# Performance work log

Measured on AMD Instinct MI355X. Metric: run time of the kernel, lower is better.

Reference implementation:

```python
import jax, jax.numpy as jnp
import numpy as np

N_EMBD = 768
N_HEAD = 12
HEAD_SIZE = N_EMBD // N_HEAD  # 64
WINDOW = 64  # sliding_window_size
EPS = 1e-6


def _rmsnorm(x, g):
    xf = x.astype(jnp.float32)
    n = xf * jax.lax.rsqrt(jnp.mean(xf * xf, axis=-1, keepdims=True) + EPS)
    return n.astype(x.dtype) * g


def _gelu_tanh(x):
    c = jnp.sqrt(jnp.asarray(2.0 / jnp.pi, x.dtype))
    return 0.5 * x * (1.0 + jnp.tanh(c * (x + 0.044715 * x ** 3)))


def setup_inputs() -> dict:
    key = jax.random.key(0)
    ks = jax.random.split(key, 12)
    B, T = 8, 1024
    s = 0.02
    return {
        "x": jax.random.normal(ks[0], (B, T, N_EMBD), jnp.float32),
        "w_q": jax.random.normal(ks[1], (N_EMBD, N_HEAD, HEAD_SIZE), jnp.float32) * s,
        "w_k": jax.random.normal(ks[2], (N_EMBD, N_HEAD, HEAD_SIZE), jnp.float32) * s,
        "w_v": jax.random.normal(ks[3], (N_EMBD, N_HEAD, HEAD_SIZE), jnp.float32) * s,
        "w_proj": jax.random.normal(ks[4], (N_EMBD, N_EMBD), jnp.float32) * s,
        "b_proj": jnp.zeros((N_EMBD,), jnp.float32),
        "w_ff1": jax.random.normal(ks[5], (N_EMBD, 4 * N_EMBD), jnp.float32) * s,
        "b_ff1": jnp.zeros((4 * N_EMBD,), jnp.float32),
        "w_ff2": jax.random.normal(ks[6], (4 * N_EMBD, N_EMBD), jnp.float32) * s,
        "b_ff2": jnp.zeros((N_EMBD,), jnp.float32),
        "g1": jnp.ones((N_EMBD,), jnp.float32),
        "g2": jnp.ones((N_EMBD,), jnp.float32),
    }


def reference(x, w_q, w_k, w_v, w_proj, b_proj, w_ff1, b_ff1, w_ff2, b_ff2, g1, g2):
    B, T, C = x.shape
    # ---- multi-head sliding-window causal attention (eval: dropout = identity) ----
    h = _rmsnorm(x, g1)
    q = jnp.einsum("btc,chd->bhtd", h, w_q)
    k = jnp.einsum("btc,chd->bhtd", h, w_k)
    v = jnp.einsum("btc,chd->bhtd", h, w_v)
    scores = jnp.einsum("bhtd,bhsd->bhts", q, k) / jnp.sqrt(jnp.asarray(HEAD_SIZE, x.dtype))
    pos = jnp.arange(T)
    diff = pos[:, None] - pos[None, :]  # q_pos - k_pos
    mask = (diff < 0) | (diff >= WINDOW)  # causal + sliding window of 64
    scores = jnp.where(mask[None, None], jnp.asarray(-jnp.inf, scores.dtype), scores)
    attn = jax.nn.softmax(scores, axis=-1)
    out = jnp.einsum("bhts,bhsd->bhtd", attn, v)
    out = out.transpose(0, 2, 1, 3).reshape(B, T, C)  # concat heads
    x = x + out @ w_proj + b_proj
    # ---- feedforward ----
    h2 = _rmsnorm(x, g2)
    ff = _gelu_tanh(h2 @ w_ff1 + b_ff1) @ w_ff2 + b_ff2
    x = x + ff
    aux = jnp.asarray(0.0, jnp.float32)
    return (x, aux)
```

## Files before the change

kernel.cpp:

```cpp
#include <hip/hip_runtime.h>
#include <cstdint>

#define DEVI __device__ __forceinline__

typedef __bf16 bf16x8 __attribute__((ext_vector_type(8)));
typedef float  f32x4  __attribute__((ext_vector_type(4)));

DEVI unsigned short f2b(float f){
  unsigned u = __builtin_bit_cast(unsigned, f);
  unsigned r = u + 0x7FFF + ((u >> 16) & 1);
  return (unsigned short)(r >> 16);
}
DEVI float b2f(unsigned short s){
  unsigned u = ((unsigned)s) << 16;
  return __builtin_bit_cast(float, u);
}
DEVI float gelu_f(float x){
  float u = 0.7978845608028654f * (x + 0.044715f * x * x * x);
  float e = __expf(2.0f * u);
  return x * (1.0f - 1.0f / (e + 1.0f));
}
DEVI void gl_lds16(const unsigned short* g, unsigned short* l){
  __builtin_amdgcn_global_load_lds(
      (const __attribute__((address_space(1))) unsigned int*)g,
      (__attribute__((address_space(3))) unsigned int*)l, 16, 0, 0);
}

__global__ __launch_bounds__(256)
void transpose_f2b(const float* __restrict__ in, unsigned short* __restrict__ out,
                   int R, int C)
{
  __shared__ float tile[32][33];
  int nbx = C >> 5;
  int bx = blockIdx.x % nbx, by = blockIdx.x / nbx;
  int c0 = bx << 5, r0 = by << 5;
  int tx = threadIdx.x & 31, ty = threadIdx.x >> 5;
  #pragma unroll
  for (int j = 0; j < 32; j += 8)
    tile[ty + j][tx] = in[(size_t)(r0 + ty + j) * C + c0 + tx];
  __syncthreads();
  #pragma unroll
  for (int j = 0; j < 32; j += 8)
    out[(size_t)(c0 + ty + j) * R + r0 + tx] = f2b(tile[tx][ty + j]);
}

__global__ __launch_bounds__(256)
void rmsnorm_k(const float* __restrict__ x, const float* __restrict__ g,
               unsigned short* __restrict__ out)
{
  int wid = threadIdx.x >> 6, lane = threadIdx.x & 63;
  size_t row = (size_t)blockIdx.x * 4 + wid;
  const float* xr = x + row * 768;
  float4 v[3];
  float ss = 0.0f;
  #pragma unroll
  for (int c = 0; c < 3; c++){
    v[c] = *(const float4*)&xr[lane * 4 + c * 256];
    ss += v[c].x * v[c].x + v[c].y * v[c].y + v[c].z * v[c].z + v[c].w * v[c].w;
  }
  #pragma unroll
  for (int o = 32; o >= 1; o >>= 1) ss += __shfl_xor(ss, o);
  float rs = rsqrtf(ss * (1.0f / 768.0f) + 1e-6f);
  #pragma unroll
  for (int c = 0; c < 3; c++){
    const float4 gv = *(const float4*)&g[lane * 4 + c * 256];
    ushort4 o4;
    o4.x = f2b(v[c].x * rs * gv.x);
    o4.y = f2b(v[c].y * rs * gv.y);
    o4.z = f2b(v[c].z * rs * gv.z);
    o4.w = f2b(v[c].w * rs * gv.w);
    *(ushort4*)&out[row * 768 + lane * 4 + c * 256] = o4;
  }
}

template<int BM, bool BIAS, bool GELU_, bool RES, bool OUTF32>
__global__ __launch_bounds__(256, BM == 64 ? 3 : 2)
void gemm_db(const unsigned short* __restrict__ A, const unsigned short* __restrict__ Bt,
             const float* __restrict__ bias, const float* __restrict__ res,
             void* __restrict__ outp, int M, int N, int K)
{
  constexpr int MI = BM / 32;
  constexpr int AL = (BM * 8) / 256;
  __shared__ unsigned short sm[2][(BM + 128) * 64];

  int tid = threadIdx.x, wid = tid >> 6, lane = tid & 63;
  int la = lane & 15, hi = lane >> 4;
  int wm = wid >> 1, wn = wid & 1;
  int tiles_n = N >> 7;
  int bid = blockIdx.x;
  bid = (bid & 7) * (gridDim.x >> 3) + (bid >> 3);
  int m0 = (bid / tiles_n) * BM, n0 = (bid % tiles_n) << 7;
  int NT = K >> 6;

  f32x4 acc[MI][4] = {};

  auto stage = [&](unsigned short* buf, int kt){
    #pragma unroll
    for (int l = 0; l < AL; l++){
      int cb  = wid * (BM * 2) + l * 64;
      int idx = cb + lane;
      int row = idx >> 3, slot = idx & 7, sl2 = slot ^ (row & 7);
      gl_lds16(A + (size_t)(m0 + row) * K + kt + sl2 * 8, buf + cb * 8);
    }
    #pragma unroll
    for (int l = 0; l < 4; l++){
      int cb  = wid * 256 + l * 64;
      int idx = cb + lane;
      int row = idx >> 3, slot = idx & 7, sl2 = slot ^ (row & 7);
      gl_lds16(Bt + (size_t)(n0 + row) * K + kt + sl2 * 8, buf + BM * 64 + cb * 8);
    }
  };

  stage(sm[0], 0);
  asm volatile("s_waitcnt vmcnt(0)" ::: "memory");
  __builtin_amdgcn_s_barrier();

  for (int t = 0; t < NT; t++){
    const unsigned short* As = sm[t & 1];
    const unsigned short* Bs = sm[t & 1] + BM * 64;

    if (t + 1 < NT) stage(sm[(t + 1) & 1], (t + 1) << 6);

    bf16x8 afr[MI][2], bfr[4][2];
    #pragma unroll
    for (int mm = 0; mm < MI; mm++)
      #pragma unroll
      for (int kk = 0; kk < 2; kk++){
        int r = wm * (BM / 2) + mm * 16 + la;
        afr[mm][kk] = *(const bf16x8*)&As[r * 64 + (((kk * 4 + hi) ^ (r & 7))) * 8];
      }
    #pragma unroll
    for (int nn = 0; nn < 4; nn++)
      #pragma unroll
      for (int kk = 0; kk < 2; kk++){
        int r = wn * 64 + nn * 16 + la;
        bfr[nn][kk] = *(const bf16x8*)&Bs[r * 64 + (((kk * 4 + hi) ^ (r & 7))) * 8];
      }
    #pragma unroll
    for (int mm = 0; mm < MI; mm++)
      #pragma unroll
      for (int nn = 0; nn < 4; nn++)
        #pragma unroll
        for (int kk = 0; kk < 2; kk++)
          acc[mm][nn] = __builtin_amdgcn_mfma_f32_16x16x32_bf16(
              afr[mm][kk], bfr[nn][kk], acc[mm][nn], 0, 0, 0);

    asm volatile("s_waitcnt vmcnt(0)" ::: "memory");
    __builtin_amdgcn_s_barrier();
  }

  float* outF = (float*)outp;
  unsigned short* outB = (unsigned short*)outp;
  #pragma unroll
  for (int mm = 0; mm < MI; mm++){
    int rowb = m0 + wm * (BM / 2) + mm * 16 + hi * 4;
    #pragma unroll
    for (int nn = 0; nn < 4; nn++){
      int col = n0 + wn * 64 + nn * 16 + la;
      float bv = BIAS ? bias[col] : 0.0f;
      #pragma unroll
      for (int r = 0; r < 4; r++){
        float val = acc[mm][nn][r] + bv;
        if (GELU_) val = gelu_f(val);
        if (RES)   val += res[(size_t)(rowb + r) * N + col];
        size_t o = (size_t)(rowb + r) * N + col;
        if (OUTF32) outF[o] = val;
        else        outB[o] = f2b(val);
      }
    }
  }
}

__global__ __launch_bounds__(256)
void attn_k(const unsigned short* __restrict__ qkv, unsigned short* __restrict__ attn)
{
  __shared__ unsigned short Qs[64 * 72];
  __shared__ unsigned short Ks[128 * 72];
  __shared__ unsigned short Vt[64 * 136];
  __shared__ unsigned short Ps[4][16 * 136];

  int tid = threadIdx.x, wid = tid >> 6, lane = tid & 63;
  int la = lane & 15, hi = lane >> 4;
  int blk = blockIdx.x;
  blk = (blk & 7) * (gridDim.x >> 3) + (blk >> 3);
  int tile = blk & 15, hb = blk >> 4;
  int h = hb % 12, b = hb / 12;
  int t0 = tile << 6;

  const unsigned short* qbase = qkv + (size_t)(b * 1024) * 2304 + h * 64;

  #pragma unroll
  for (int r = 0; r < 2; r++){
    int idx = tid + r * 256;
    int row = idx >> 3, ch = idx & 7;
    uint4 v = *(const uint4*)(qbase + (size_t)(t0 + row) * 2304 + ch * 8);
    *(uint4*)&Qs[row * 72 + ch * 8] = v;
  }
  #pragma unroll
  for (int r = 0; r < 4; r++){
    int idx = tid + r * 256;
    int row = idx >> 3, ch = idx & 7;
    int sg = t0 - 64 + row; sg = sg < 0 ? 0 : sg;
    uint4 v = *(const uint4*)(qbase + 768 + (size_t)sg * 2304 + ch * 8);
    *(uint4*)&Ks[row * 72 + ch * 8] = v;
  }
  #pragma unroll
  for (int r = 0; r < 4; r++){
    int idx = tid + r * 256;
    int s = idx & 127, ch = idx >> 7;
    int sg = t0 - 64 + s; sg = sg < 0 ? 0 : sg;
    uint4 v = *(const uint4*)(qbase + 1536 + (size_t)sg * 2304 + ch * 8);
    unsigned short tmp[8];
    *(uint4*)tmp = v;
    #pragma unroll
    for (int j = 0; j < 8; j++)
      Vt[(ch * 8 + j) * 136 + s] = tmp[j];
  }
  __syncthreads();

  f32x4 sc[8];
  #pragma unroll
  for (int sj = 0; sj < 8; sj++) sc[sj] = (f32x4){0.f, 0.f, 0.f, 0.f};
  #pragma unroll
  for (int kk = 0; kk < 2; kk++){
    bf16x8 aq = *(const bf16x8*)&Qs[(wid * 16 + la) * 72 + kk * 32 + hi * 8];
    #pragma unroll
    for (int sj = 0; sj < 8; sj++){
      bf16x8 bk = *(const bf16x8*)&Ks[(sj * 16 + la) * 72 + kk * 32 + hi * 8];
      sc[sj] = __builtin_amdgcn_mfma_f32_16x16x32_bf16(aq, bk, sc[sj], 0, 0, 0);
    }
  }

  float inv[4];
  #pragma unroll
  for (int r2 = 0; r2 < 4; r2++){
    int row = wid * 16 + hi * 4 + r2;
    float mx = -1e30f;
    #pragma unroll
    for (int sj = 0; sj < 8; sj++){
      int sl = sj * 16 + la;
      bool valid = (sl >= row + 1) && (sl <= row + 64) && (t0 - 64 + sl >= 0);
      float sv = valid ? sc[sj][r2] * 0.125f : -1e30f;
      sc[sj][r2] = sv;
      mx = fmaxf(mx, sv);
    }
    #pragma unroll
    for (int o = 8; o >= 1; o >>= 1) mx = fmaxf(mx, __shfl_xor(mx, o));
    float sum = 0.0f;
    #pragma unroll
    for (int sj = 0; sj < 8; sj++){
      float p = __expf(sc[sj][r2] - mx);
      sc[sj][r2] = p;
      sum += p;
    }
    #pragma unroll
    for (int o = 8; o >= 1; o >>= 1) sum += __shfl_xor(sum, o);
    inv[r2] = 1.0f / sum;
  }

  unsigned short* myP = Ps[wid];
  #pragma unroll
  for (int sj = 0; sj < 8; sj++)
    #pragma unroll
    for (int r2 = 0; r2 < 4; r2++)
      myP[(hi * 4 + r2) * 136 + sj * 16 + la] = f2b(sc[sj][r2]);

  __syncthreads();

  f32x4 oacc[4];
  #pragma unroll
  for (int nj = 0; nj < 4; nj++) oacc[nj] = (f32x4){0.f, 0.f, 0.f, 0.f};
  #pragma unroll
  for (int ks = 0; ks < 4; ks++){
    bf16x8 ap = *(const bf16x8*)&myP[la * 136 + ks * 32 + hi * 8];
    #pragma unroll
    for (int nj = 0; nj < 4; nj++){
      bf16x8 bv = *(const bf16x8*)&Vt[(nj * 16 + la) * 136 + ks * 32 + hi * 8];
      oacc[nj] = __builtin_amdgcn_mfma_f32_16x16x32_bf16(ap, bv, oacc[nj], 0, 0, 0);
    }
  }

  unsigned short* obase = attn + (size_t)(b * 1024 + t0) * 768 + h * 64;
  #pragma unroll
  for (int nj = 0; nj < 4; nj++)
    #pragma unroll
    for (int r2 = 0; r2 < 4; r2++){
      int row = wid * 16 + hi * 4 + r2;
      obase[(size_t)row * 768 + nj * 16 + la] = f2b(oacc[nj][r2] * inv[r2]);
    }
}

__global__ void aux_k(float* p){ if (threadIdx.x == 0) p[0] = 0.0f; }

extern "C" void kernel_launch(void* const* d_in, const int* in_sizes, int n_in,
                              void* d_out, int out_size, void* d_ws, size_t ws_size,
                              hipStream_t stream)
{
  const float* x      = (const float*)d_in[0];
  const float* w_q    = (const float*)d_in[1];
  const float* w_k    = (const float*)d_in[2];
  const float* w_v    = (const float*)d_in[3];
  const float* w_proj = (const float*)d_in[4];
  const float* b_proj = (const float*)d_in[5];
  const float* w_ff1  = (const float*)d_in[6];
  const float* b_ff1  = (const float*)d_in[7];
  const float* w_ff2  = (const float*)d_in[8];
  const float* b_ff2  = (const float*)d_in[9];
  const float* g1     = (const float*)d_in[10];
  const float* g2     = (const float*)d_in[11];
  float* out = (float*)d_out;

  char* ws = (char*)d_ws;
  size_t off = 0;
  auto alloc = [&](size_t bytes){ size_t r = off; off += (bytes + 255) & ~(size_t)255; return r; };
  const size_t BT = 8 * 1024;

  unsigned short* h     = (unsigned short*)(ws + alloc(BT * 768 * 2));
  unsigned short* qkv   = (unsigned short*)(ws + alloc(BT * 3072 * 2));
  float*          x2    = (float*)         (ws + alloc(BT * 768 * 4));
  unsigned short* h2    = (unsigned short*)(ws + alloc(BT * 768 * 2));
  unsigned short* WqkvT = (unsigned short*)(ws + alloc(2304 * 768 * 2));
  unsigned short* WprojT= (unsigned short*)(ws + alloc(768 * 768 * 2));
  unsigned short* Wff1T = (unsigned short*)(ws + alloc(3072 * 768 * 2));
  unsigned short* Wff2T = (unsigned short*)(ws + alloc(768 * 3072 * 2));
  unsigned short* attn  = h;
  unsigned short* ffa   = qkv;

  transpose_f2b<<<576, 256, 0, stream>>>(w_q,    WqkvT,             768, 768);
  transpose_f2b<<<576, 256, 0, stream>>>(w_k,    WqkvT + 768 * 768, 768, 768);
  transpose_f2b<<<576, 256, 0, stream>>>(w_v,    WqkvT + 1536 * 768,768, 768);
  transpose_f2b<<<576, 256, 0, stream>>>(w_proj, WprojT,            768, 768);
  transpose_f2b<<<24 * 96, 256, 0, stream>>>(w_ff1, Wff1T, 768, 3072);
  transpose_f2b<<<96 * 24, 256, 0, stream>>>(w_ff2, Wff2T, 3072, 768);

  rmsnorm_k<<<2048, 256, 0, stream>>>(x, g1, h);

  gemm_db<128,false,false,false,false><<<64 * 18, 256, 0, stream>>>(h, WqkvT, nullptr, nullptr, qkv, 8192, 2304, 768);

  attn_k<<<8 * 12 * 16, 256, 0, stream>>>(qkv, attn);

  gemm_db<64,true,false,true,true><<<128 * 6, 256, 0, stream>>>(attn, WprojT, b_proj, x, x2, 8192, 768, 768);

  rmsnorm_k<<<2048, 256, 0, stream>>>(x2, g2, h2);

  gemm_db<128,true,true,false,false><<<64 * 24, 256, 0, stream>>>(h2, Wff1T, b_ff1, nullptr, ffa, 8192, 3072, 768);

  gemm_db<64,true,false,true,true><<<128 * 6, 256, 0, stream>>>(ffa, Wff2T, b_ff2, x2, out, 8192, 768, 3072);

  aux_k<<<1, 64, 0, stream>>>(out + 6291456);
}
```

Measured before the change: 228.9 us.

## Replace double-buffered GEMM with triple-buffered 128x192 tile GEMM

```diff
diff --git a/kernel.cpp b/kernel.cpp
--- a/kernel.cpp
+++ b/kernel.cpp
@@ -73,90 +73,93 @@
   }
 }
 
-template<int BM, bool BIAS, bool GELU_, bool RES, bool OUTF32>
-__global__ __launch_bounds__(256, BM == 64 ? 3 : 2)
-void gemm_db(const unsigned short* __restrict__ A, const unsigned short* __restrict__ Bt,
-             const float* __restrict__ bias, const float* __restrict__ res,
-             void* __restrict__ outp, int M, int N, int K)
-{
-  constexpr int MI = BM / 32;
-  constexpr int AL = (BM * 8) / 256;
-  __shared__ unsigned short sm[2][(BM + 128) * 64];
+template<bool BIAS, bool GELU_, bool RES, bool OUTF32>
+__global__ __launch_bounds__(256, 1)
+void gemm_tri(const unsigned short* __restrict__ A, const unsigned short* __restrict__ Bt,
+              const float* __restrict__ bias, const float* __restrict__ res,
+              void* __restrict__ outp, int M, int N, int K)
+{
+  constexpr int NF = 6;
+  constexpr int RSZ = (128 + 192) * 64;
+  __shared__ unsigned short sm[3][RSZ];
 
   int tid = threadIdx.x, wid = tid >> 6, lane = tid & 63;
   int la = lane & 15, hi = lane >> 4;
   int wm = wid >> 1, wn = wid & 1;
-  int tiles_n = N >> 7;
+  int tiles_n = N / 192;
   int bid = blockIdx.x;
   bid = (bid & 7) * (gridDim.x >> 3) + (bid >> 3);
-  int m0 = (bid / tiles_n) * BM, n0 = (bid % tiles_n) << 7;
+  int m0 = (bid / tiles_n) * 128, n0 = (bid % tiles_n) * 192;
   int NT = K >> 6;
 
-  f32x4 acc[MI][4] = {};
+  f32x4 acc[4][NF] = {};
 
   auto stage = [&](unsigned short* buf, int kt){
     #pragma unroll
-    for (int l = 0; l < AL; l++){
-      int cb  = wid * (BM * 2) + l * 64;
+    for (int l = 0; l < 4; l++){
+      int cb = wid * 256 + l * 64;
       int idx = cb + lane;
-      int row = idx >> 3, slot = idx & 7, sl2 = slot ^ (row & 7);
+      int row = idx >> 3, sl2 = (idx & 7) ^ (row & 7);
       gl_lds16(A + (size_t)(m0 + row) * K + kt + sl2 * 8, buf + cb * 8);
     }
     #pragma unroll
-    for (int l = 0; l < 4; l++){
-      int cb  = wid * 256 + l * 64;
+    for (int l = 0; l < 6; l++){
+      int cb = wid * 384 + l * 64;
       int idx = cb + lane;
-      int row = idx >> 3, slot = idx & 7, sl2 = slot ^ (row & 7);
-      gl_lds16(Bt + (size_t)(n0 + row) * K + kt + sl2 * 8, buf + BM * 64 + cb * 8);
+      int row = idx >> 3, sl2 = (idx & 7) ^ (row & 7);
+      gl_lds16(Bt + (size_t)(n0 + row) * K + kt + sl2 * 8, buf + 8192 + cb * 8);
     }
   };
 
+  auto compute = [&](const unsigned short* buf){
+    const unsigned short* As = buf;
+    const unsigned short* Bs = buf + 8192;
+    #pragma unroll
+    for (int kk = 0; kk < 2; kk++){
+      bf16x8 afr[4], bfr[NF];
+      #pragma unroll
+      for (int mm = 0; mm < 4; mm++){
+        int r = wm * 64 + mm * 16 + la;
+        afr[mm] = *(const bf16x8*)&As[r * 64 + ((kk * 4 + hi) ^ (r & 7)) * 8];
+      }
+      #pragma unroll
+      for (int nn = 0; nn < NF; nn++){
+        int r = wn * 96 + nn * 16 + la;
+        bfr[nn] = *(const bf16x8*)&Bs[r * 64 + ((kk * 4 + hi) ^ (r & 7)) * 8];
+      }
+      #pragma unroll
+      for (int mm = 0; mm < 4; mm++)
+        #pragma unroll
+        for (int nn = 0; nn < NF; nn++)
+          acc[mm][nn] = __builtin_amdgcn_mfma_f32_16x16x32_bf16(
+              afr[mm], bfr[nn], acc[mm][nn], 0, 0, 0);
+    }
+  };
+
   stage(sm[0], 0);
-  asm volatile("s_waitcnt vmcnt(0)" ::: "memory");
-  __builtin_amdgcn_s_barrier();
-
+  stage(sm[1], 64);
+
+  int cur = 0;
   for (int t = 0; t < NT; t++){
-    const unsigned short* As = sm[t & 1];
-    const unsigned short* Bs = sm[t & 1] + BM * 64;
-
-    if (t + 1 < NT) stage(sm[(t + 1) & 1], (t + 1) << 6);
-
-    bf16x8 afr[MI][2], bfr[4][2];
-    #pragma unroll
-    for (int mm = 0; mm < MI; mm++)
-      #pragma unroll
-      for (int kk = 0; kk < 2; kk++){
-        int r = wm * (BM / 2) + mm * 16 + la;
-        afr[mm][kk] = *(const bf16x8*)&As[r * 64 + (((kk * 4 + hi) ^ (r & 7))) * 8];
-      }
-    #pragma unroll
-    for (int nn = 0; nn < 4; nn++)
-      #pragma unroll
-      for (int kk = 0; kk < 2; kk++){
-        int r = wn * 64 + nn * 16 + la;
-        bfr[nn][kk] = *(const bf16x8*)&Bs[r * 64 + (((kk * 4 + hi) ^ (r & 7))) * 8];
-      }
-    #pragma unroll
-    for (int mm = 0; mm < MI; mm++)
-      #pragma unroll
-      for (int nn = 0; nn < 4; nn++)
-        #pragma unroll
-        for (int kk = 0; kk < 2; kk++)
-          acc[mm][nn] = __builtin_amdgcn_mfma_f32_16x16x32_bf16(
-              afr[mm][kk], bfr[nn][kk], acc[mm][nn], 0, 0, 0);
-
-    asm volatile("s_waitcnt vmcnt(0)" ::: "memory");
+    if (t + 2 < NT)
+      stage(sm[cur + 2 >= 3 ? cur - 1 : cur + 2], (t + 2) << 6);
+    if (t + 2 < NT)      asm volatile("s_waitcnt vmcnt(20)" ::: "memory");
+    else if (t + 1 < NT) asm volatile("s_waitcnt vmcnt(10)" ::: "memory");
+    else                 asm volatile("s_waitcnt vmcnt(0)"  ::: "memory");
     __builtin_amdgcn_s_barrier();
+    compute(sm[cur]);
+    __builtin_amdgcn_s_barrier();
+    cur = (cur == 2) ? 0 : cur + 1;
   }
 
   float* outF = (float*)outp;
   unsigned short* outB = (unsigned short*)outp;
   #pragma unroll
-  for (int mm = 0; mm < MI; mm++){
-    int rowb = m0 + wm * (BM / 2) + mm * 16 + hi * 4;
-    #pragma unroll
-    for (int nn = 0; nn < 4; nn++){
-      int col = n0 + wn * 64 + nn * 16 + la;
+  for (int mm = 0; mm < 4; mm++){
+    int rowb = m0 + wm * 64 + mm * 16 + hi * 4;
+    #pragma unroll
+    for (int nn = 0; nn < NF; nn++){
+      int col = n0 + wn * 96 + nn * 16 + la;
       float bv = BIAS ? bias[col] : 0.0f;
       #pragma unroll
       for (int r = 0; r < 4; r++){
@@ -335,17 +338,17 @@
 
   rmsnorm_k<<<2048, 256, 0, stream>>>(x, g1, h);
 
-  gemm_db<128,false,false,false,false><<<64 * 18, 256, 0, stream>>>(h, WqkvT, nullptr, nullptr, qkv, 8192, 2304, 768);
+  gemm_tri<false,false,false,false><<<768, 256, 0, stream>>>(h, WqkvT, nullptr, nullptr, qkv, 8192, 2304, 768);
 
   attn_k<<<8 * 12 * 16, 256, 0, stream>>>(qkv, attn);
 
-  gemm_db<64,true,false,true,true><<<128 * 6, 256, 0, stream>>>(attn, WprojT, b_proj, x, x2, 8192, 768, 768);
+  gemm_tri<true,false,true,true><<<256, 256, 0, stream>>>(attn, WprojT, b_proj, x, x2, 8192, 768, 768);
 
   rmsnorm_k<<<2048, 256, 0, stream>>>(x2, g2, h2);
 
-  gemm_db<128,true,true,false,false><<<64 * 24, 256, 0, stream>>>(h2, Wff1T, b_ff1, nullptr, ffa, 8192, 3072, 768);
-
-  gemm_db<64,true,false,true,true><<<128 * 6, 256, 0, stream>>>(ffa, Wff2T, b_ff2, x2, out, 8192, 768, 3072);
+  gemm_tri<true,true,false,false><<<1024, 256, 0, stream>>>(h2, Wff1T, b_ff1, nullptr, ffa, 8192, 3072, 768);
+
+  gemm_tri<true,false,true,true><<<256, 256, 0, stream>>>(ffa, Wff2T, b_ff2, x2, out, 8192, 768, 3072);
 
   aux_k<<<1, 64, 0, stream>>>(out + 6291456);
 }
```

Result: no change. 232.8 us (+1.7%).
